# Optimization experiments

Measured on AMD Instinct MI355X. Metric: run time of the kernel, lower is better.

Reference implementation:

```python
import jax, jax.numpy as jnp
from jax import lax
import numpy as np

T, I, H, H2 = 2048, 64, 256, 1024  # time steps, input feats, hidden, hidden2


def _lstm(x, Wih, Whh, bih, bhh):
    """PyTorch-convention LSTM. x: [T, B, I]; Wih: [4H, I]; Whh: [4H, H].
    Gate order i, f, g, o. Returns hidden states [T, B, H]."""
    Hd = Whh.shape[1]
    b = bih + bhh
    xw = jnp.einsum('tbi,gi->tbg', x, Wih) + b  # precompute input projections

    def step(carry, xt):
        h, c = carry
        z = xt + h @ Whh.T
        i, f, g, o = jnp.split(z, 4, axis=-1)
        c = jax.nn.sigmoid(f) * c + jax.nn.sigmoid(i) * jnp.tanh(g)
        h = jax.nn.sigmoid(o) * jnp.tanh(c)
        return (h, c), h

    h0 = jnp.zeros((x.shape[1], Hd), x.dtype)
    _, hs = lax.scan(step, (h0, h0), xw)
    return hs


def setup_inputs() -> dict:
    key = jax.random.key(0)
    ks = jax.random.split(key, 16)
    s1 = 1.0 / np.sqrt(H)
    s2 = 1.0 / np.sqrt(H2)
    d = {
        'x': jax.random.normal(ks[0], (T, I, 21), jnp.float32),
        'Wih1': jax.random.uniform(ks[1], (4 * H, I), jnp.float32, -s1, s1),
        'Whh1': jax.random.uniform(ks[2], (4 * H, H), jnp.float32, -s1, s1),
        'bih1': jax.random.uniform(ks[3], (4 * H,), jnp.float32, -s1, s1),
        'bhh1': jax.random.uniform(ks[4], (4 * H,), jnp.float32, -s1, s1),
        'Wih2': jax.random.uniform(ks[5], (4 * H2, H * 21), jnp.float32, -s2, s2),
        'Whh2': jax.random.uniform(ks[6], (4 * H2, H2), jnp.float32, -s2, s2),
        'bih2': jax.random.uniform(ks[7], (4 * H2,), jnp.float32, -s2, s2),
        'bhh2': jax.random.uniform(ks[8], (4 * H2,), jnp.float32, -s2, s2),
        'Wih3': jax.random.uniform(ks[9], (4 * H, H2), jnp.float32, -s1, s1),
        'Whh3': jax.random.uniform(ks[10], (4 * H, H), jnp.float32, -s1, s1),
        'bih3': jax.random.uniform(ks[11], (4 * H,), jnp.float32, -s1, s1),
        'bhh3': jax.random.uniform(ks[12], (4 * H,), jnp.float32, -s1, s1),
        'Wfc': jax.random.uniform(ks[13], (21, H), jnp.float32, -s1, s1),
        'bfc': jax.random.uniform(ks[14], (21,), jnp.float32, -s1, s1),
    }
    return d


def reference(x, Wih1, Whh1, bih1, bhh1, Wih2, Whh2, bih2, bhh2,
              Wih3, Whh3, bih3, bhh3, Wfc, bfc):
    # The 21-iteration torch loop runs lstm1 independently on each of the 21
    # channel slices with batch=1; fold the 21 channels into the batch dim.
    x1 = jnp.transpose(x, (0, 2, 1))           # [T, 21, I]
    h1 = _lstm(x1, Wih1, Whh1, bih1, bhh1)     # [T, 21, H]
    # x_torch[:, :, i*H:(i+1)*H] = channel i -> channel-major concat
    xcat = h1.reshape(T, 1, 21 * H)            # [T, 1, 21H]
    h2 = _lstm(xcat, Wih2, Whh2, bih2, bhh2)   # [T, 1, H2]
    h3 = _lstm(h2, Wih3, Whh3, bih3, bhh3)     # [T, 1, H]
    out = h3 @ Wfc.T + bfc                     # [T, 1, 21]
    return out
```

## Files before the change

### kernel.cpp

```cpp
#include <hip/hip_runtime.h>


#define T_STEPS 2048
#define SENT 0xFFFFFFFFu

using f4v   = __attribute__((ext_vector_type(4))) float;
using s8v   = __attribute__((ext_vector_type(8))) short;
using u16x8 = __attribute__((ext_vector_type(8))) unsigned short;
using u32x4 = __attribute__((ext_vector_type(4))) unsigned;

__device__ __forceinline__ unsigned short f2bf(float v) {
  unsigned u = __float_as_uint(v);
  u = (u + 0x7FFFu + ((u >> 16) & 1u)) >> 16;
  return (unsigned short)u;
}
__device__ __forceinline__ float bf2f(unsigned short b) {
  return __uint_as_float(((unsigned)b) << 16);
}
__device__ __forceinline__ unsigned packhl(float v) {
  unsigned short hb = f2bf(v);
  unsigned short lb = f2bf(v - bf2f(hb));
  return (((unsigned)hb) << 16) | lb;
}
__device__ __forceinline__ float unpackhl(unsigned p) {
  return __uint_as_float(p & 0xFFFF0000u) + __uint_as_float(p << 16);
}
__device__ __forceinline__ float sigm(float x) { return 1.0f / (1.0f + __expf(-x)); }
__device__ __forceinline__ float tanh_f(float x) {
  float ax = fabsf(x);
  float e = __expf(-2.0f * ax);
  float t = (1.0f - e) / (1.0f + e);
  return copysignf(t, x);
}
__device__ __forceinline__ unsigned ld_agent32(const unsigned* p) {
  return __hip_atomic_load(p, __ATOMIC_RELAXED, __HIP_MEMORY_SCOPE_AGENT);
}
__device__ __forceinline__ void st_agent32(unsigned* p, unsigned v) {
  __hip_atomic_store(p, v, __ATOMIC_RELAXED, __HIP_MEMORY_SCOPE_AGENT);
}
__device__ __forceinline__ void ctr_add(unsigned* p) {
  __hip_atomic_fetch_add(p, 1u, __ATOMIC_RELAXED, __HIP_MEMORY_SCOPE_AGENT);
}
__device__ __forceinline__ void poll_ctr(const unsigned* p, unsigned tgt) {
  unsigned n = 0;
  while (ld_agent32(p) < tgt) {
    if (++n > (1u << 22)) break;
    __builtin_amdgcn_s_sleep(4);
  }
}
template <int N_>
__device__ __forceinline__ void poll_sent(const unsigned* p, int lane, unsigned* c) {
#pragma unroll
  for (int k = 0; k < N_; ++k) c[k] = ld_agent32(p + 64 * k + lane);
  unsigned n = 0;
  for (;;) {
    bool ok = true;
#pragma unroll
    for (int k = 0; k < N_; ++k) ok &= (c[k] != SENT);
    if (ok || ++n > (1u << 20)) break;
    __builtin_amdgcn_s_sleep(1);
#pragma unroll
    for (int k = 0; k < N_; ++k) c[k] = ld_agent32(p + 64 * k + lane);
  }
}
#define VMCNT0() asm volatile("s_waitcnt vmcnt(0)" ::: "memory")

#define L16(M) M(0) M(1) M(2) M(3) M(4) M(5) M(6) M(7) M(8) M(9) M(10) M(11) \
  M(12) M(13) M(14) M(15)
#define L64(M) L16(M) M(16) M(17) M(18) M(19) M(20) M(21) M(22) M(23) M(24) \
  M(25) M(26) M(27) M(28) M(29) M(30) M(31) M(32) M(33) M(34) M(35) M(36) \
  M(37) M(38) M(39) M(40) M(41) M(42) M(43) M(44) M(45) M(46) M(47) M(48) \
  M(49) M(50) M(51) M(52) M(53) M(54) M(55) M(56) M(57) M(58) M(59) M(60) \
  M(61) M(62) M(63)

__device__ __forceinline__ void unpack8(u32x4 a, u32x4 b, u16x8& hi, u16x8& lo) {
#pragma unroll
  for (int j = 0; j < 4; ++j) {
    hi[j]     = (unsigned short)(a[j] >> 16);
    lo[j]     = (unsigned short)(a[j] & 0xFFFFu);
    hi[4 + j] = (unsigned short)(b[j] >> 16);
    lo[4 + j] = (unsigned short)(b[j] & 0xFFFFu);
  }
}

__device__ void gemm_tile_packed(
    const unsigned* __restrict__ Ap, const unsigned short* __restrict__ Bh,
    const unsigned short* __restrict__ Bl, const float* __restrict__ b1,
    const float* __restrict__ b2, unsigned* __restrict__ C,
    int tm, int tn, int K, int N, char* smem)
{
  unsigned short* lds = (unsigned short*)smem;
  const size_t m0 = (size_t)tm * 128, n0 = (size_t)tn * 128;
  const int tid = threadIdx.x, lane = tid & 63, w = tid >> 6;
  const int wr = w >> 1, wc = w & 1;
  const int srow = tid >> 2, sc8 = (tid & 3) * 8;

  const unsigned* pA = Ap + m0 * K;
  const unsigned short* pBh = Bh + n0 * K;
  const unsigned short* pBl = Bl + n0 * K;

  f4v acc[4][4];
#pragma unroll
  for (int i = 0; i < 4; ++i)
#pragma unroll
    for (int j = 0; j < 4; ++j) acc[i][j] = f4v{0.f, 0.f, 0.f, 0.f};

  u32x4 a00, a01, a10, a11;
  u16x8 s4, s5, s6, s7;
#define LOADK(k0)                                                           \
  a00 = *(const u32x4*)(pA + (size_t)srow * K + (k0) + sc8);                \
  a01 = *(const u32x4*)(pA + (size_t)srow * K + (k0) + sc8 + 4);            \
  a10 = *(const u32x4*)(pA + (size_t)(srow + 64) * K + (k0) + sc8);         \
  a11 = *(const u32x4*)(pA + (size_t)(srow + 64) * K + (k0) + sc8 + 4);     \
  s4 = *(const u16x8*)(pBh + (size_t)srow * K + (k0) + sc8);                \
  s5 = *(const u16x8*)(pBh + (size_t)(srow + 64) * K + (k0) + sc8);         \
  s6 = *(const u16x8*)(pBl + (size_t)srow * K + (k0) + sc8);                \
  s7 = *(const u16x8*)(pBl + (size_t)(srow + 64) * K + (k0) + sc8);

  LOADK(0);
  const int fr = lane & 15, fko = (lane >> 4) * 8;
  for (int k0 = 0; k0 < K; k0 += 32) {
    u16x8 h0, l0, h1, l1;
    unpack8(a00, a01, h0, l0);
    unpack8(a10, a11, h1, l1);
    *(u16x8*)&lds[0     +  srow       * 32 + sc8] = h0;
    *(u16x8*)&lds[0     + (srow + 64) * 32 + sc8] = h1;
    *(u16x8*)&lds[4096  +  srow       * 32 + sc8] = l0;
    *(u16x8*)&lds[4096  + (srow + 64) * 32 + sc8] = l1;
    *(u16x8*)&lds[8192  +  srow       * 32 + sc8] = s4;
    *(u16x8*)&lds[8192  + (srow + 64) * 32 + sc8] = s5;
    *(u16x8*)&lds[12288 +  srow       * 32 + sc8] = s6;
    *(u16x8*)&lds[12288 + (srow + 64) * 32 + sc8] = s7;
    __syncthreads();
    if (k0 + 32 < K) { LOADK(k0 + 32); }
    s8v afh[4], afl[4], bfh[4], bfl[4];
#pragma unroll
    for (int i = 0; i < 4; ++i) {
      int ar = (64 * wr + 16 * i + fr) * 32 + fko;
      int br = (64 * wc + 16 * i + fr) * 32 + fko;
      afh[i] = *(const s8v*)&lds[0 + ar];
      afl[i] = *(const s8v*)&lds[4096 + ar];
      bfh[i] = *(const s8v*)&lds[8192 + br];
      bfl[i] = *(const s8v*)&lds[12288 + br];
    }
#pragma unroll
    for (int mi = 0; mi < 4; ++mi)
#pragma unroll
      for (int ni = 0; ni < 4; ++ni) {
        acc[mi][ni] = __builtin_amdgcn_mfma_f32_16x16x32_bf16(afh[mi], bfh[ni], acc[mi][ni], 0, 0, 0);
        acc[mi][ni] = __builtin_amdgcn_mfma_f32_16x16x32_bf16(afh[mi], bfl[ni], acc[mi][ni], 0, 0, 0);
        acc[mi][ni] = __builtin_amdgcn_mfma_f32_16x16x32_bf16(afl[mi], bfh[ni], acc[mi][ni], 0, 0, 0);
      }
    __syncthreads();
  }
#undef LOADK
  const int er = (lane >> 4) * 4, ec = lane & 15;
#pragma unroll
  for (int ni = 0; ni < 4; ++ni) {
    size_t col = n0 + 64 * wc + 16 * ni + ec;
    float bv = b1[col] + b2[col];
#pragma unroll
    for (int mi = 0; mi < 4; ++mi) {
      size_t row = m0 + 64 * wr + 16 * mi + er;
#pragma unroll
      for (int rr = 0; rr < 4; ++rr)
        st_agent32(&C[(row + rr) * N + col], __float_as_uint(acc[mi][ni][rr] + bv));
    }
  }
}

__global__ __launch_bounds__(256, 1) void mega_kernel(
    const float* __restrict__ x,
    const float* __restrict__ Wih1, const float* __restrict__ Whh1,
    const float* __restrict__ bih1, const float* __restrict__ bhh1,
    const float* __restrict__ Whh2,
    const float* __restrict__ bih2, const float* __restrict__ bhh2,
    const float* __restrict__ Whh3,
    const float* __restrict__ bih3, const float* __restrict__ bhh3,
    unsigned* __restrict__ h1r0, unsigned* __restrict__ h2r0,
    unsigned* __restrict__ h3r0, unsigned* __restrict__ cnt,
    unsigned* __restrict__ h1rows, unsigned* __restrict__ h2rows,
    unsigned* __restrict__ h3rows,
    float* __restrict__ xw2, float* __restrict__ xw3,
    const unsigned short* __restrict__ wih2h, const unsigned short* __restrict__ wih2l,
    const unsigned short* __restrict__ wih3h, const unsigned short* __restrict__ wih3l)
{
  __shared__ __align__(16) char smem[32768];
  unsigned* ready1 = cnt + 0;
  unsigned* done2  = cnt + 16;
  unsigned* ready2 = cnt + 32;
  unsigned* done3  = cnt + 48;
  const int wg = blockIdx.x;
  const int widx = threadIdx.x >> 6, lane = threadIdx.x & 63;

  if (wg < 84) {
    const int c = wg / 4, sub = wg % 4;
    const int gwv = sub * 4 + widx;
    const int u16i = lane & 15, g = lane >> 4;
    const int grow = g * 256 + gwv * 16 + u16i;

    const f4v* wsrc = (const f4v*)(Whh1 + (size_t)grow * 256);
    const f4v* xsrc = (const f4v*)(Wih1 + (size_t)grow * 64);
#define DH(i) f4v m##i = wsrc[i];
#define DX(i) f4v n##i = xsrc[i];
    L64(DH)
    L16(DX)
#undef DH
#undef DX
    const float bias = bih1[grow] + bhh1[grow];

    float* xls = (float*)smem;
    float* hbb = (float*)(smem + 1024);
    float* const xq = xls + widx * 64;
    float* const hb0 = hbb + widx * 512;

    float cst = 0.0f;
    float xpre = x[(size_t)lane * 21 + c];

    for (int t = 0; t < T_STEPS; ++t) {
      xq[lane] = xpre;
      if (t + 1 < T_STEPS) xpre = x[(size_t)(t + 1) * 1344 + lane * 21 + c];
      const unsigned* src = t ? h1rows + (size_t)(t - 1) * 5376 + c * 256
                              : h1r0 + c * 256;
      unsigned cv[4];
      poll_sent<4>(src, lane, cv);
      float* hb = hb0 + (t & 1) * 256;
      hb[lane]       = unpackhl(cv[0]);
      hb[64 + lane]  = unpackhl(cv[1]);
      hb[128 + lane] = unpackhl(cv[2]);
      hb[192 + lane] = unpackhl(cv[3]);
      float a0 = 0, a1 = 0, a2 = 0, a3 = 0;
#define FH(i) { f4v h4 = *(const f4v*)&hb[4 * i]; \
  a0 = fmaf(m##i[0], h4[0], a0); a1 = fmaf(m##i[1], h4[1], a1); \
  a2 = fmaf(m##i[2], h4[2], a2); a3 = fmaf(m##i[3], h4[3], a3); }
#define FX(i) { f4v x4 = *(const f4v*)&xq[4 * i]; \
  a0 = fmaf(n##i[0], x4[0], a0); a1 = fmaf(n##i[1], x4[1], a1); \
  a2 = fmaf(n##i[2], x4[2], a2); a3 = fmaf(n##i[3], x4[3], a3); }
      L64(FH)
      L16(FX)
#undef FH
#undef FX
      float z = (a0 + a1) + (a2 + a3) + bias;
      float zi = __shfl(z, u16i);
      float zf = __shfl(z, 16 + u16i);
      float zg = __shfl(z, 32 + u16i);
      float zo = __shfl(z, 48 + u16i);
      if (lane < 16) {
        float cn = sigm(zf) * cst + sigm(zi) * tanh_f(zg);
        float hn = sigm(zo) * tanh_f(cn);
        cst = cn;
        st_agent32(&h1rows[(size_t)t * 5376 + c * 256 + gwv * 16 + lane], packhl(hn));
      }
      if ((t & 127) == 127) {
        VMCNT0();
        if (lane == 0) ctr_add(&ready1[t >> 7]);
      }
    }
  } else if (wg < 148) {
    const int gw = (wg - 84) * 4 + widx;
    const int q = lane >> 4, r4 = lane & 15;
    const int u = r4 & 3, g = r4 >> 2;
    const int grow = g * 1024 + gw * 4 + u;

    const f4v* wsrc = (const f4v*)(Whh2 + (size_t)grow * 1024 + q * 256);
#define DW(i) f4v w##i = wsrc[i];
    L64(DW)
#undef DW

    float* hs = (float*)smem;
    float cst = 0.0f;
    float xwn = 0.0f;

    for (int t = 0; t < T_STEPS; ++t) {
      float xwv;
      if ((t & 127) == 0) {
        poll_ctr(&done2[t >> 7], 32);
        xwv = xw2[(size_t)t * 4096 + grow];
      } else xwv = xwn;
      float* hsb = hs + (t & 1) * 1040;
      if (widx == 0) {
        const unsigned* src = t ? h2rows + (size_t)(t - 1) * 1024 : h2r0;
        unsigned cv[16];
        poll_sent<16>(src, lane, cv);
#pragma unroll
        for (int k = 0; k < 16; ++k)
          hsb[(k >> 2) * 260 + (k & 3) * 64 + lane] = unpackhl(cv[k]);
      }
      __syncthreads();
      const float* qreg = hsb + q * 260;
      float a0 = 0, a1 = 0, a2 = 0, a3 = 0;
#define FW(i) { f4v h4 = *(const f4v*)&qreg[4 * i]; \
  a0 = fmaf(w##i[0], h4[0], a0); a1 = fmaf(w##i[1], h4[1], a1); \
  a2 = fmaf(w##i[2], h4[2], a2); a3 = fmaf(w##i[3], h4[3], a3); }
      L64(FW)
#undef FW
      float z = (a0 + a1) + (a2 + a3);
      z += __shfl_xor(z, 16);
      z += __shfl_xor(z, 32);
      z += xwv;
      float zi  = __shfl(z, u);
      float zf  = __shfl(z, 4 + u);
      float zg2 = __shfl(z, 8 + u);
      float zo  = __shfl(z, 12 + u);
      if (lane < 4) {
        float cn = sigm(zf) * cst + sigm(zi) * tanh_f(zg2);
        float hn = sigm(zo) * tanh_f(cn);
        cst = cn;
        st_agent32(&h2rows[(size_t)t * 1024 + gw * 4 + lane], packhl(hn));
      }
      if ((t & 127) == 127) {
        VMCNT0();
        if (lane == 0) ctr_add(&ready2[t >> 7]);
      }
      if (t + 1 < T_STEPS && ((t + 1) & 127) != 0)
        xwn = xw2[(size_t)(t + 1) * 4096 + grow];
    }
  } else if (wg < 152) {
    const int gw = (wg - 148) * 4 + widx;
    const int u16i = lane & 15, g = lane >> 4;
    const int grow = g * 256 + gw * 16 + u16i;

    const f4v* wsrc = (const f4v*)(Whh3 + (size_t)grow * 256);
#define DW(i) f4v w##i = wsrc[i];
    L64(DW)
#undef DW

    float* hbb = (float*)smem;
    float* const hb0 = hbb + widx * 512;
    float cst = 0.0f;
    float xwn = 0.0f;

    for (int t = 0; t < T_STEPS; ++t) {
      float xwv;
      if ((t & 127) == 0) {
        poll_ctr(&done3[t >> 7], 8);
        xwv = xw3[(size_t)t * 1024 + grow];
      } else xwv = xwn;
      const unsigned* src = t ? h3rows + (size_t)(t - 1) * 256 : h3r0;
      unsigned cv[4];
      poll_sent<4>(src, lane, cv);
      float* hb = hb0 + (t & 1) * 256;
      hb[lane]       = __uint_as_float(cv[0]);
      hb[64 + lane]  = __uint_as_float(cv[1]);
      hb[128 + lane] = __uint_as_float(cv[2]);
      hb[192 + lane] = __uint_as_float(cv[3]);
      float a0 = 0, a1 = 0, a2 = 0, a3 = 0;
#define FW(i) { f4v h4 = *(const f4v*)&hb[4 * i]; \
  a0 = fmaf(w##i[0], h4[0], a0); a1 = fmaf(w##i[1], h4[1], a1); \
  a2 = fmaf(w##i[2], h4[2], a2); a3 = fmaf(w##i[3], h4[3], a3); }
      L64(FW)
#undef FW
      float z = (a0 + a1) + (a2 + a3) + xwv;
      float zi = __shfl(z, u16i);
      float zf = __shfl(z, 16 + u16i);
      float zg = __shfl(z, 32 + u16i);
      float zo = __shfl(z, 48 + u16i);
      if (lane < 16) {
        float cn = sigm(zf) * cst + sigm(zi) * tanh_f(zg);
        float hn = sigm(zo) * tanh_f(cn);
        cst = cn;
        st_agent32(&h3rows[(size_t)t * 256 + gw * 16 + lane], __float_as_uint(hn));
      }
      if (t + 1 < T_STEPS && ((t + 1) & 127) != 0)
        xwn = xw3[(size_t)(t + 1) * 1024 + grow];
    }
  } else if (wg < 206) {
    const int pw = wg - 152;
    for (int i = pw; i < 512; i += 54) {
      int tm = i >> 5, tn = i & 31;
      poll_ctr(&ready1[tm], 336);
      gemm_tile_packed(h1rows, wih2h, wih2l, bih2, bhh2,
                       (unsigned*)xw2, tm, tn, 5376, 4096, smem);
      VMCNT0();
      __syncthreads();
      if (threadIdx.x == 0) ctr_add(&done2[tm]);
      __syncthreads();
    }
  } else {
    const int pw = wg - 206;
    for (int i = pw; i < 128; i += 14) {
      int tm = i >> 3, tn = i & 7;
      poll_ctr(&ready2[tm], 256);
      gemm_tile_packed(h2rows, wih3h, wih3l, bih3, bhh3,
                       (unsigned*)xw3, tm, tn, 1024, 1024, smem);
      VMCNT0();
      __syncthreads();
      if (threadIdx.x == 0) ctr_add(&done3[tm]);
      __syncthreads();
    }
  }
}

__global__ void split_kernel(const float* __restrict__ src,
                             unsigned short* __restrict__ hi,
                             unsigned short* __restrict__ lo, int n) {
  int i = blockIdx.x * 256 + threadIdx.x;
  if (i < n) {
    float v = src[i];
    unsigned short hb = f2bf(v);
    hi[i] = hb;
    lo[i] = f2bf(v - bf2f(hb));
  }
}

__global__ void fc_kernel(const float* __restrict__ h3, const float* __restrict__ Wfc,
                          const float* __restrict__ bfc, float* __restrict__ out) {
  int t = blockIdx.x, m = threadIdx.x;
  if (m < 21) {
    const float* hp = h3 + (size_t)t * 256;
    const float* wp = Wfc + m * 256;
    float a = 0.0f;
#pragma unroll 8
    for (int j = 0; j < 256; ++j) a = fmaf(wp[j], hp[j], a);
    out[t * 21 + m] = a + bfc[m];
  }
}

extern "C" void kernel_launch(void* const* d_in, const int* in_sizes, int n_in,
                              void* d_out, int out_size, void* d_ws, size_t ws_size,
                              hipStream_t stream) {
  const float* x    = (const float*)d_in[0];
  const float* Wih1 = (const float*)d_in[1];
  const float* Whh1 = (const float*)d_in[2];
  const float* bih1 = (const float*)d_in[3];
  const float* bhh1 = (const float*)d_in[4];
  const float* Wih2 = (const float*)d_in[5];
  const float* Whh2 = (const float*)d_in[6];
  const float* bih2 = (const float*)d_in[7];
  const float* bhh2 = (const float*)d_in[8];
  const float* Wih3 = (const float*)d_in[9];
  const float* Whh3 = (const float*)d_in[10];
  const float* bih3 = (const float*)d_in[11];
  const float* bhh3 = (const float*)d_in[12];
  const float* Wfc  = (const float*)d_in[13];
  const float* bfc  = (const float*)d_in[14];
  float* out = (float*)d_out;

  const size_t WS_NEEDED = 188776448;
  if (ws_size < WS_NEEDED) return;
  char* ws = (char*)d_ws;
  unsigned* h1r0 = (unsigned*)(ws + 0);
  unsigned* h2r0 = (unsigned*)(ws + 21504);
  unsigned* h3r0 = (unsigned*)(ws + 25600);
  unsigned* cnt  = (unsigned*)(ws + 26624);
  unsigned* h1rows = (unsigned*)(ws + 32768);
  unsigned* h2rows = (unsigned*)(ws + 44072960);
  unsigned* h3rows = (unsigned*)(ws + 52461568);
  float* xw2 = (float*)(ws + 54558720);
  float* xw3 = (float*)(ws + 88113152);
  unsigned short* wih2h = (unsigned short*)(ws + 96501760);
  unsigned short* wih2l = (unsigned short*)(ws + 140541952);
  unsigned short* wih3h = (unsigned short*)(ws + 184582144);
  unsigned short* wih3l = (unsigned short*)(ws + 186679296);

  hipMemsetAsync(ws, 0, 32768, stream);
  hipMemsetAsync(ws + 32768, 0xFF, 54525952, stream);

  const int nW2 = 4096 * 5376;
  split_kernel<<<(nW2 + 255) / 256, 256, 0, stream>>>(Wih2, wih2h, wih2l, nW2);
  const int nW3 = 1024 * 1024;
  split_kernel<<<(nW3 + 255) / 256, 256, 0, stream>>>(Wih3, wih3h, wih3l, nW3);

  mega_kernel<<<220, 256, 0, stream>>>(
      x, Wih1, Whh1, bih1, bhh1,
      Whh2, bih2, bhh2, Whh3, bih3, bhh3,
      h1r0, h2r0, h3r0, cnt,
      h1rows, h2rows, h3rows, xw2, xw3,
      wih2h, wih2l, wih3h, wih3l);

  fc_kernel<<<2048, 64, 0, stream>>>((const float*)h3rows, Wfc, bfc, out);
}
```

Measured before the change: 9.880 ms.

## Poll recurrent state with vectorized coherent loads and drop LSTM2 block barrier

Replaces the per-dword sentinel polling loop with 16-byte global loads that use sc0 sc1 cache bits and spin without sleeping. Each wave now writes four contiguous floats per lane into LDS. In the LSTM2 section every wave polls and unpacks the hidden state into its own LDS copy, which removes the __syncthreads that used to follow wave 0's load. Single-buffered per-wave LDS replaces the double buffer. This lowers handoff latency on the serial recurrence, at the cost of more polling traffic and redundant loads across waves.

```diff
diff --git a/kernel.cpp b/kernel.cpp
--- a/kernel.cpp
+++ b/kernel.cpp
@@ -48,20 +48,12 @@
     __builtin_amdgcn_s_sleep(4);
   }
 }
-template <int N_>
-__device__ __forceinline__ void poll_sent(const unsigned* p, int lane, unsigned* c) {
-#pragma unroll
-  for (int k = 0; k < N_; ++k) c[k] = ld_agent32(p + 64 * k + lane);
-  unsigned n = 0;
-  for (;;) {
-    bool ok = true;
-#pragma unroll
-    for (int k = 0; k < N_; ++k) ok &= (c[k] != SENT);
-    if (ok || ++n > (1u << 20)) break;
-    __builtin_amdgcn_s_sleep(1);
-#pragma unroll
-    for (int k = 0; k < N_; ++k) c[k] = ld_agent32(p + 64 * k + lane);
-  }
+__device__ __forceinline__ u32x4 ld16_coh(const unsigned* addr) {
+  u32x4 c;
+  asm volatile("global_load_dwordx4 %0, %1, off sc0 sc1\n\t"
+               "s_waitcnt vmcnt(0)"
+               : "=&v"(c) : "v"(addr) : "memory");
+  return c;
 }
 #define VMCNT0() asm volatile("s_waitcnt vmcnt(0)" ::: "memory")
 
@@ -209,10 +201,8 @@
 #undef DX
     const float bias = bih1[grow] + bhh1[grow];
 
-    float* xls = (float*)smem;
-    float* hbb = (float*)(smem + 1024);
-    float* const xq = xls + widx * 64;
-    float* const hb0 = hbb + widx * 512;
+    float* const hb = (float*)smem + widx * 320;
+    float* const xq = hb + 256;
 
     float cst = 0.0f;
     float xpre = x[(size_t)lane * 21 + c];
@@ -222,13 +212,17 @@
       if (t + 1 < T_STEPS) xpre = x[(size_t)(t + 1) * 1344 + lane * 21 + c];
       const unsigned* src = t ? h1rows + (size_t)(t - 1) * 5376 + c * 256
                               : h1r0 + c * 256;
-      unsigned cv[4];
-      poll_sent<4>(src, lane, cv);
-      float* hb = hb0 + (t & 1) * 256;
-      hb[lane]       = unpackhl(cv[0]);
-      hb[64 + lane]  = unpackhl(cv[1]);
-      hb[128 + lane] = unpackhl(cv[2]);
-      hb[192 + lane] = unpackhl(cv[3]);
+      const unsigned* addr = src + 4 * lane;
+      u32x4 c0;
+      unsigned n = 0;
+      for (;;) {
+        c0 = ld16_coh(addr);
+        bool ok = (c0[0] != SENT) && (c0[1] != SENT) &&
+                  (c0[2] != SENT) && (c0[3] != SENT);
+        if (ok || ++n > (1u << 18)) break;
+      }
+      *(f4v*)&hb[4 * lane] = f4v{unpackhl(c0[0]), unpackhl(c0[1]),
+                                 unpackhl(c0[2]), unpackhl(c0[3])};
       float a0 = 0, a1 = 0, a2 = 0, a3 = 0;
 #define FH(i) { f4v h4 = *(const f4v*)&hb[4 * i]; \
   a0 = fmaf(m##i[0], h4[0], a0); a1 = fmaf(m##i[1], h4[1], a1); \
@@ -267,7 +261,9 @@
     L64(DW)
 #undef DW
 
-    float* hs = (float*)smem;
+    float* const wls = (float*)smem + widx * 1040;
+    const float* const qreg = wls + q * 260;
+
     float cst = 0.0f;
     float xwn = 0.0f;
 
@@ -277,17 +273,32 @@
         poll_ctr(&done2[t >> 7], 32);
         xwv = xw2[(size_t)t * 4096 + grow];
       } else xwv = xwn;
-      float* hsb = hs + (t & 1) * 1040;
-      if (widx == 0) {
+      {
         const unsigned* src = t ? h2rows + (size_t)(t - 1) * 1024 : h2r0;
-        unsigned cv[16];
-        poll_sent<16>(src, lane, cv);
-#pragma unroll
-        for (int k = 0; k < 16; ++k)
-          hsb[(k >> 2) * 260 + (k & 3) * 64 + lane] = unpackhl(cv[k]);
-      }
-      __syncthreads();
-      const float* qreg = hsb + q * 260;
+        const unsigned* addr = src + 4 * lane;
+        u32x4 c0, c1, c2, c3;
+        unsigned n = 0;
+        for (;;) {
+          asm volatile(
+              "global_load_dwordx4 %0, %4, off sc0 sc1\n\t"
+              "global_load_dwordx4 %1, %4, off offset:1024 sc0 sc1\n\t"
+              "global_load_dwordx4 %2, %4, off offset:2048 sc0 sc1\n\t"
+              "global_load_dwordx4 %3, %4, off offset:3072 sc0 sc1\n\t"
+              "s_waitcnt vmcnt(0)"
+              : "=&v"(c0), "=&v"(c1), "=&v"(c2), "=&v"(c3)
+              : "v"(addr) : "memory");
+          bool ok = true;
+#pragma unroll
+          for (int j = 0; j < 4; ++j)
+            ok = ok && (c0[j] != SENT) && (c1[j] != SENT) &&
+                       (c2[j] != SENT) && (c3[j] != SENT);
+          if (ok || ++n > (1u << 18)) break;
+        }
+        *(f4v*)&wls[0 * 260 + 4 * lane] = f4v{unpackhl(c0[0]), unpackhl(c0[1]), unpackhl(c0[2]), unpackhl(c0[3])};
+        *(f4v*)&wls[1 * 260 + 4 * lane] = f4v{unpackhl(c1[0]), unpackhl(c1[1]), unpackhl(c1[2]), unpackhl(c1[3])};
+        *(f4v*)&wls[2 * 260 + 4 * lane] = f4v{unpackhl(c2[0]), unpackhl(c2[1]), unpackhl(c2[2]), unpackhl(c2[3])};
+        *(f4v*)&wls[3 * 260 + 4 * lane] = f4v{unpackhl(c3[0]), unpackhl(c3[1]), unpackhl(c3[2]), unpackhl(c3[3])};
+      }
       float a0 = 0, a1 = 0, a2 = 0, a3 = 0;
 #define FW(i) { f4v h4 = *(const f4v*)&qreg[4 * i]; \
   a0 = fmaf(w##i[0], h4[0], a0); a1 = fmaf(w##i[1], h4[1], a1); \
@@ -325,8 +336,7 @@
     L64(DW)
 #undef DW
 
-    float* hbb = (float*)smem;
-    float* const hb0 = hbb + widx * 512;
+    float* const hb = (float*)smem + widx * 256;
     float cst = 0.0f;
     float xwn = 0.0f;
 
@@ -337,13 +347,17 @@
         xwv = xw3[(size_t)t * 1024 + grow];
       } else xwv = xwn;
       const unsigned* src = t ? h3rows + (size_t)(t - 1) * 256 : h3r0;
-      unsigned cv[4];
-      poll_sent<4>(src, lane, cv);
-      float* hb = hb0 + (t & 1) * 256;
-      hb[lane]       = __uint_as_float(cv[0]);
-      hb[64 + lane]  = __uint_as_float(cv[1]);
-      hb[128 + lane] = __uint_as_float(cv[2]);
-      hb[192 + lane] = __uint_as_float(cv[3]);
+      const unsigned* addr = src + 4 * lane;
+      u32x4 c0;
+      unsigned n = 0;
+      for (;;) {
+        c0 = ld16_coh(addr);
+        bool ok = (c0[0] != SENT) && (c0[1] != SENT) &&
+                  (c0[2] != SENT) && (c0[3] != SENT);
+        if (ok || ++n > (1u << 18)) break;
+      }
+      *(f4v*)&hb[4 * lane] = f4v{__uint_as_float(c0[0]), __uint_as_float(c0[1]),
+                                 __uint_as_float(c0[2]), __uint_as_float(c0[3])};
       float a0 = 0, a1 = 0, a2 = 0, a3 = 0;
 #define FW(i) { f4v h4 = *(const f4v*)&hb[4 * i]; \
   a0 = fmaf(w##i[0], h4[0], a0); a1 = fmaf(w##i[1], h4[1], a1); \
```

Result: no change. 9.738 ms (-1.4%).
